# Kernel optimization log

Hardware: AMD Instinct MI355X
Metric: run time of the kernel (lower is better)

## Reference

```python
import jax, jax.numpy as jnp
import numpy as np


def _wkv(time_decay, time_first, k, v):
    # time_decay, time_first: [C]; k, v: [B, T, C]
    w = -jnp.exp(time_decay)  # per-channel decay (negative)
    u = time_first
    B, T, C = k.shape
    aa = jnp.zeros((B, C), dtype=k.dtype)
    bb = jnp.zeros((B, C), dtype=k.dtype)
    pp = jnp.full((B, C), -1e38, dtype=k.dtype)  # running max exponent

    def step(carry, kv_t):
        aa, bb, pp = carry
        kt, vt = kv_t  # [B, C] each
        # output with bonus u for current token
        ww = u + kt
        q = jnp.maximum(pp, ww)
        e1 = jnp.exp(pp - q)
        e2 = jnp.exp(ww - q)
        y_t = (e1 * aa + e2 * vt) / (e1 * bb + e2)
        # decayed state update
        ww2 = pp + w
        q2 = jnp.maximum(ww2, kt)
        e1b = jnp.exp(ww2 - q2)
        e2b = jnp.exp(kt - q2)
        new_carry = (e1b * aa + e2b * vt, e1b * bb + e2b, q2)
        return new_carry, y_t

    ks = jnp.transpose(k, (1, 0, 2))  # [T, B, C]
    vs = jnp.transpose(v, (1, 0, 2))
    _, ys = jax.lax.scan(step, (aa, bb, pp), (ks, vs))
    return jnp.transpose(ys, (1, 0, 2))  # [B, T, C]


def setup_inputs() -> dict:
    key = jax.random.key(0)
    k1, k2, k3, k4 = jax.random.split(key, 4)
    B, T, C = 8, 1024, 2048
    return {
        "batch_size": B,
        "seq_len": T,
        "embedding_dim": C,
        "time_decay": jax.random.normal(k1, (C,), dtype=jnp.float32),
        "time_first": jax.random.normal(k2, (C,), dtype=jnp.float32),
        "k": jax.random.normal(k3, (B, T, C), dtype=jnp.float32),
        "v": jax.random.normal(k4, (B, T, C), dtype=jnp.float32),
    }


def reference(batch_size, seq_len, embedding_dim, time_decay, time_first, k, v):
    assert seq_len <= 1024  # T_max
    return _wkv(time_decay, time_first, k, v)
```

## Files before the change

### kernel.cpp

```cpp
#include <hip/hip_runtime.h>


#define T_FIX 1024
#define NCH   32
#define CHL   (T_FIX / NCH)
#define BATCH 8

__device__ __forceinline__ void wkv_step(float& aa, float& bb, float& pp,
                                         float w, float kt, float vt)
{
    float ww2 = pp + w;
    float q2  = fmaxf(ww2, kt);
    float e1  = __expf(ww2 - q2);
    float e2  = __expf(kt - q2);
    aa = fmaf(e1, aa, e2 * vt);
    bb = fmaf(e1, bb, e2);
    pp = q2;
}

#define F4TOA(a, f) { a[0] = (f).x; a[1] = (f).y; a[2] = (f).z; a[3] = (f).w; }

__global__ __launch_bounds__(256)
void wkv_states(const float* __restrict__ td,
                const float* __restrict__ k,
                const float* __restrict__ v,
                float* __restrict__ aa_s,
                float* __restrict__ bb_s,
                float* __restrict__ pp_s,
                int B, int C)
{
    const int C4  = C >> 2;
    int gid = blockIdx.x * blockDim.x + threadIdx.x;
    if (gid >= B * NCH * C4) return;
    int c4  = gid % C4;
    int rem = gid / C4;
    int j   = rem % NCH;
    int b   = rem / NCH;
    int c   = c4 << 2;

    float4 tdv = *(const float4*)(td + c);
    float w[4] = { -__expf(tdv.x), -__expf(tdv.y), -__expf(tdv.z), -__expf(tdv.w) };

    const size_t base = ((size_t)b * T_FIX + (size_t)j * CHL) * C + c;
    const float* kp = k + base;
    const float* vp = v + base;

    float aa[4] = {0.f, 0.f, 0.f, 0.f};
    float bb[4] = {0.f, 0.f, 0.f, 0.f};
    float pp[4] = {-1e38f, -1e38f, -1e38f, -1e38f};

    for (int tb = 0; tb < CHL; tb += BATCH) {
        float4 kb[BATCH], vb[BATCH];
        #pragma unroll
        for (int i = 0; i < BATCH; ++i) {
            kb[i] = *(const float4*)(kp + (size_t)(tb + i) * C);
            vb[i] = *(const float4*)(vp + (size_t)(tb + i) * C);
        }
        #pragma unroll
        for (int i = 0; i < BATCH; ++i) {
            float ka[4], va[4];
            F4TOA(ka, kb[i]); F4TOA(va, vb[i]);
            #pragma unroll
            for (int cc = 0; cc < 4; ++cc)
                wkv_step(aa[cc], bb[cc], pp[cc], w[cc], ka[cc], va[cc]);
        }
    }

    size_t sidx = ((size_t)j * B + b) * C + c;
    *(float4*)(aa_s + sidx) = make_float4(aa[0], aa[1], aa[2], aa[3]);
    *(float4*)(bb_s + sidx) = make_float4(bb[0], bb[1], bb[2], bb[3]);
    *(float4*)(pp_s + sidx) = make_float4(pp[0], pp[1], pp[2], pp[3]);
}

__global__ __launch_bounds__(256)
void wkv_emit(const float* __restrict__ td,
              const float* __restrict__ tf,
              const float* __restrict__ k,
              const float* __restrict__ v,
              const float* __restrict__ aa_s,
              const float* __restrict__ bb_s,
              const float* __restrict__ pp_s,
              float* __restrict__ y,
              int B, int C)
{
    const int C4  = C >> 2;
    int gid = blockIdx.x * blockDim.x + threadIdx.x;
    if (gid >= B * NCH * C4) return;
    int c4  = gid % C4;
    int rem = gid / C4;
    int j   = rem % NCH;
    int b   = rem / NCH;
    int c   = c4 << 2;

    float4 tdv = *(const float4*)(td + c);
    float4 tfv = *(const float4*)(tf + c);
    float w[4] = { -__expf(tdv.x), -__expf(tdv.y), -__expf(tdv.z), -__expf(tdv.w) };
    float u[4];  F4TOA(u, tfv);

    float aa[4] = {0.f, 0.f, 0.f, 0.f};
    float bb[4] = {0.f, 0.f, 0.f, 0.f};
    float pp[4] = {-1e38f, -1e38f, -1e38f, -1e38f};

    for (int jj = 0; jj < j; ++jj) {
        size_t sidx = ((size_t)jj * B + b) * C + c;
        float4 c_a = *(const float4*)(aa_s + sidx);
        float4 c_b = *(const float4*)(bb_s + sidx);
        float4 c_m = *(const float4*)(pp_s + sidx);
        float ca[4], cb[4], cm[4];
        F4TOA(ca, c_a); F4TOA(cb, c_b); F4TOA(cm, c_m);
        #pragma unroll
        for (int cc = 0; cc < 4; ++cc) {
            float ppd = pp[cc] + (float)CHL * w[cc];
            float pn  = fmaxf(ppd, cm[cc]);
            float ea  = __expf(ppd - pn);
            float eb  = __expf(cm[cc] - pn);
            aa[cc] = fmaf(ea, aa[cc], eb * ca[cc]);
            bb[cc] = fmaf(ea, bb[cc], eb * cb[cc]);
            pp[cc] = pn;
        }
    }

    const size_t base = ((size_t)b * T_FIX + (size_t)j * CHL) * C + c;
    const float* kp = k + base;
    const float* vp = v + base;
    float*       yp = y + base;

    for (int tb = 0; tb < CHL; tb += BATCH) {
        float4 kb[BATCH], vb[BATCH];
        #pragma unroll
        for (int i = 0; i < BATCH; ++i) {
            kb[i] = *(const float4*)(kp + (size_t)(tb + i) * C);
            vb[i] = *(const float4*)(vp + (size_t)(tb + i) * C);
        }
        #pragma unroll
        for (int i = 0; i < BATCH; ++i) {
            float ka[4], va[4], ya[4];
            F4TOA(ka, kb[i]); F4TOA(va, vb[i]);
            #pragma unroll
            for (int cc = 0; cc < 4; ++cc) {
                float ww = u[cc] + ka[cc];
                float q  = fmaxf(pp[cc], ww);
                float e1 = __expf(pp[cc] - q);
                float e2 = __expf(ww - q);
                ya[cc] = __fdividef(fmaf(e1, aa[cc], e2 * va[cc]),
                                    fmaf(e1, bb[cc], e2));
                wkv_step(aa[cc], bb[cc], pp[cc], w[cc], ka[cc], va[cc]);
            }
            *(float4*)(yp + (size_t)(tb + i) * C) = make_float4(ya[0], ya[1], ya[2], ya[3]);
        }
    }
}

extern "C" void kernel_launch(void* const* d_in, const int* in_sizes, int n_in,
                              void* d_out, int out_size, void* d_ws, size_t ws_size,
                              hipStream_t stream)
{
    const float* td = (const float*)d_in[3];
    const float* tf = (const float*)d_in[4];
    const float* k  = (const float*)d_in[5];
    const float* v  = (const float*)d_in[6];
    float*       y  = (float*)d_out;

    const int C   = in_sizes[3];
    const int BTC = in_sizes[5];
    const int B   = BTC / (T_FIX * C);

    const size_t N = (size_t)B * C * NCH;
    float* aa_s = (float*)d_ws;
    float* bb_s = aa_s + N;
    float* pp_s = bb_s + N;

    const int block   = 256;
    const int threads = B * NCH * (C >> 2);
    const int grid    = (threads + block - 1) / block;

    wkv_states<<<grid, block, 0, stream>>>(td, k, v, aa_s, bb_s, pp_s, B, C);
    wkv_emit  <<<grid, block, 0, stream>>>(td, tf, k, v, aa_s, bb_s, pp_s, y, B, C);
}
```

Measured before the change: 214.7 us.

## Add separate chunk-prefix scan kernel, double chunk count, use base-2 exponentials

Inserts a third kernel that scans the per-chunk states sequentially once per (batch, channel) and writes exclusive prefix states back in place. The emit kernel then loads its starting state directly instead of redoing an O(j) combine loop over all earlier chunks. The chunk count doubles to 64, giving more parallel threads and shorter serial chains per chunk. Exponentials are rescaled into base 2 so they map to exp2. The trade-off is an extra launch and a small serial scan kernel with low thread count.

```diff
diff --git a/kernel.cpp b/kernel.cpp
--- a/kernel.cpp
+++ b/kernel.cpp
@@ -1,18 +1,20 @@
 #include <hip/hip_runtime.h>
 
 
-#define T_FIX 1024
-#define NCH   32
-#define CHL   (T_FIX / NCH)
-#define BATCH 8
-
-__device__ __forceinline__ void wkv_step(float& aa, float& bb, float& pp,
-                                         float w, float kt, float vt)
-{
-    float ww2 = pp + w;
-    float q2  = fmaxf(ww2, kt);
-    float e1  = __expf(ww2 - q2);
-    float e2  = __expf(kt - q2);
+#define T_FIX  1024
+#define NCH    64
+#define CHL    (T_FIX / NCH)
+#define BATCH  8
+#define SBATCH 8
+#define L2E    1.4426950408889634f
+
+__device__ __forceinline__ void wkv_step2(float& aa, float& bb, float& pp,
+                                          float w2, float k2, float vt)
+{
+    float ww2 = pp + w2;
+    float q2  = fmaxf(ww2, k2);
+    float e1  = exp2f(ww2 - q2);
+    float e2  = exp2f(k2 - q2);
     aa = fmaf(e1, aa, e2 * vt);
     bb = fmaf(e1, bb, e2);
     pp = q2;
@@ -39,7 +41,8 @@
     int c   = c4 << 2;
 
     float4 tdv = *(const float4*)(td + c);
-    float w[4] = { -__expf(tdv.x), -__expf(tdv.y), -__expf(tdv.z), -__expf(tdv.w) };
+    float w2[4] = { -__expf(tdv.x) * L2E, -__expf(tdv.y) * L2E,
+                    -__expf(tdv.z) * L2E, -__expf(tdv.w) * L2E };
 
     const size_t base = ((size_t)b * T_FIX + (size_t)j * CHL) * C + c;
     const float* kp = k + base;
@@ -62,7 +65,7 @@
             F4TOA(ka, kb[i]); F4TOA(va, vb[i]);
             #pragma unroll
             for (int cc = 0; cc < 4; ++cc)
-                wkv_step(aa[cc], bb[cc], pp[cc], w[cc], ka[cc], va[cc]);
+                wkv_step2(aa[cc], bb[cc], pp[cc], w2[cc], ka[cc] * L2E, va[cc]);
         }
     }
 
@@ -70,6 +73,61 @@
     *(float4*)(aa_s + sidx) = make_float4(aa[0], aa[1], aa[2], aa[3]);
     *(float4*)(bb_s + sidx) = make_float4(bb[0], bb[1], bb[2], bb[3]);
     *(float4*)(pp_s + sidx) = make_float4(pp[0], pp[1], pp[2], pp[3]);
+}
+
+__global__ __launch_bounds__(256)
+void wkv_scan(const float* __restrict__ td,
+              float* __restrict__ aa_s,
+              float* __restrict__ bb_s,
+              float* __restrict__ pp_s,
+              int B, int C)
+{
+    const int C4 = C >> 2;
+    int gid = blockIdx.x * blockDim.x + threadIdx.x;
+    if (gid >= B * C4) return;
+    int c4 = gid % C4;
+    int b  = gid / C4;
+    int c  = c4 << 2;
+
+    float4 tdv = *(const float4*)(td + c);
+    float wL[4] = { -__expf(tdv.x) * (L2E * (float)CHL),
+                    -__expf(tdv.y) * (L2E * (float)CHL),
+                    -__expf(tdv.z) * (L2E * (float)CHL),
+                    -__expf(tdv.w) * (L2E * (float)CHL) };
+
+    float aa[4] = {0.f, 0.f, 0.f, 0.f};
+    float bb[4] = {0.f, 0.f, 0.f, 0.f};
+    float pp[4] = {-1e38f, -1e38f, -1e38f, -1e38f};
+
+    for (int jb = 0; jb < NCH; jb += SBATCH) {
+        float4 ca4[SBATCH], cb4[SBATCH], cm4[SBATCH];
+        #pragma unroll
+        for (int i = 0; i < SBATCH; ++i) {
+            size_t sidx = ((size_t)(jb + i) * B + b) * C + c;
+            ca4[i] = *(const float4*)(aa_s + sidx);
+            cb4[i] = *(const float4*)(bb_s + sidx);
+            cm4[i] = *(const float4*)(pp_s + sidx);
+        }
+        #pragma unroll
+        for (int i = 0; i < SBATCH; ++i) {
+            size_t sidx = ((size_t)(jb + i) * B + b) * C + c;
+            *(float4*)(aa_s + sidx) = make_float4(aa[0], aa[1], aa[2], aa[3]);
+            *(float4*)(bb_s + sidx) = make_float4(bb[0], bb[1], bb[2], bb[3]);
+            *(float4*)(pp_s + sidx) = make_float4(pp[0], pp[1], pp[2], pp[3]);
+            float ca[4], cb[4], cm[4];
+            F4TOA(ca, ca4[i]); F4TOA(cb, cb4[i]); F4TOA(cm, cm4[i]);
+            #pragma unroll
+            for (int cc = 0; cc < 4; ++cc) {
+                float ppd = pp[cc] + wL[cc];
+                float pn  = fmaxf(ppd, cm[cc]);
+                float ea  = exp2f(ppd - pn);
+                float eb  = exp2f(cm[cc] - pn);
+                aa[cc] = fmaf(ea, aa[cc], eb * ca[cc]);
+                bb[cc] = fmaf(ea, bb[cc], eb * cb[cc]);
+                pp[cc] = pn;
+            }
+        }
+    }
 }
 
 __global__ __launch_bounds__(256)
@@ -94,31 +152,16 @@
 
     float4 tdv = *(const float4*)(td + c);
     float4 tfv = *(const float4*)(tf + c);
-    float w[4] = { -__expf(tdv.x), -__expf(tdv.y), -__expf(tdv.z), -__expf(tdv.w) };
-    float u[4];  F4TOA(u, tfv);
-
-    float aa[4] = {0.f, 0.f, 0.f, 0.f};
-    float bb[4] = {0.f, 0.f, 0.f, 0.f};
-    float pp[4] = {-1e38f, -1e38f, -1e38f, -1e38f};
-
-    for (int jj = 0; jj < j; ++jj) {
-        size_t sidx = ((size_t)jj * B + b) * C + c;
-        float4 c_a = *(const float4*)(aa_s + sidx);
-        float4 c_b = *(const float4*)(bb_s + sidx);
-        float4 c_m = *(const float4*)(pp_s + sidx);
-        float ca[4], cb[4], cm[4];
-        F4TOA(ca, c_a); F4TOA(cb, c_b); F4TOA(cm, c_m);
-        #pragma unroll
-        for (int cc = 0; cc < 4; ++cc) {
-            float ppd = pp[cc] + (float)CHL * w[cc];
-            float pn  = fmaxf(ppd, cm[cc]);
-            float ea  = __expf(ppd - pn);
-            float eb  = __expf(cm[cc] - pn);
-            aa[cc] = fmaf(ea, aa[cc], eb * ca[cc]);
-            bb[cc] = fmaf(ea, bb[cc], eb * cb[cc]);
-            pp[cc] = pn;
-        }
-    }
+    float w2[4] = { -__expf(tdv.x) * L2E, -__expf(tdv.y) * L2E,
+                    -__expf(tdv.z) * L2E, -__expf(tdv.w) * L2E };
+    float u2[4] = { tfv.x * L2E, tfv.y * L2E, tfv.z * L2E, tfv.w * L2E };
+
+    size_t sidx = ((size_t)j * B + b) * C + c;
+    float4 a4 = *(const float4*)(aa_s + sidx);
+    float4 b4 = *(const float4*)(bb_s + sidx);
+    float4 p4 = *(const float4*)(pp_s + sidx);
+    float aa[4], bb[4], pp[4];
+    F4TOA(aa, a4); F4TOA(bb, b4); F4TOA(pp, p4);
 
     const size_t base = ((size_t)b * T_FIX + (size_t)j * CHL) * C + c;
     const float* kp = k + base;
@@ -138,13 +181,14 @@
             F4TOA(ka, kb[i]); F4TOA(va, vb[i]);
             #pragma unroll
             for (int cc = 0; cc < 4; ++cc) {
-                float ww = u[cc] + ka[cc];
+                float k2 = ka[cc] * L2E;
+                float ww = u2[cc] + k2;
                 float q  = fmaxf(pp[cc], ww);
-                float e1 = __expf(pp[cc] - q);
-                float e2 = __expf(ww - q);
+                float e1 = exp2f(pp[cc] - q);
+                float e2 = exp2f(ww - q);
                 ya[cc] = __fdividef(fmaf(e1, aa[cc], e2 * va[cc]),
                                     fmaf(e1, bb[cc], e2));
-                wkv_step(aa[cc], bb[cc], pp[cc], w[cc], ka[cc], va[cc]);
+                wkv_step2(aa[cc], bb[cc], pp[cc], w2[cc], k2, va[cc]);
             }
             *(float4*)(yp + (size_t)(tb + i) * C) = make_float4(ya[0], ya[1], ya[2], ya[3]);
         }
@@ -170,10 +214,15 @@
     float* bb_s = aa_s + N;
     float* pp_s = bb_s + N;
 
-    const int block   = 256;
-    const int threads = B * NCH * (C >> 2);
-    const int grid    = (threads + block - 1) / block;
-
-    wkv_states<<<grid, block, 0, stream>>>(td, k, v, aa_s, bb_s, pp_s, B, C);
-    wkv_emit  <<<grid, block, 0, stream>>>(td, tf, k, v, aa_s, bb_s, pp_s, y, B, C);
-}
+    const int block = 256;
+
+    const int threadsA = B * NCH * (C >> 2);
+    const int gridA    = (threadsA + block - 1) / block;
+
+    const int threadsS = B * (C >> 2);
+    const int gridS    = (threadsS + block - 1) / block;
+
+    wkv_states<<<gridA, block, 0, stream>>>(td, k, v, aa_s, bb_s, pp_s, B, C);
+    wkv_scan  <<<gridS, block, 0, stream>>>(td, aa_s, bb_s, pp_s, B, C);
+    wkv_emit  <<<gridA, block, 0, stream>>>(td, tf, k, v, aa_s, bb_s, pp_s, y, B, C);
+}
```

Measured after the change: 232.0 us. +8.1%, slower.
